# Performance work log

Hardware: AMD Instinct MI355X
Metric: run time of the kernel (lower is better)

Reference implementation:

```python
import jax, jax.numpy as jnp
import numpy as np

B, N, M = 2, 2048, 1024
C, CTX, H = 1024, 1024, 16
D = C // H
HID = int(C * 4.0)
EPS = 1e-6


def _ln(h):
    # LayerNorm32: fp32 layernorm, eps=1e-6, no affine params
    h32 = h.astype(jnp.float32)
    mu = jnp.mean(h32, axis=-1, keepdims=True)
    var = jnp.var(h32, axis=-1, keepdims=True)
    return ((h32 - mu) * jax.lax.rsqrt(var + EPS)).astype(h.dtype)


def _sdpa(q, k, v):
    # q: [B,Q,H,D], k/v: [B,K,H,D]
    scale = 1.0 / np.sqrt(D)
    s = jnp.einsum('bqhd,bkhd->bhqk', q, k) * scale
    p = jax.nn.softmax(s, axis=-1)
    return jnp.einsum('bhqk,bkhd->bqhd', p, v)


def _forward(x, context, Wqkv, bqkv, Wos, bos, Wq, bq, Wkv, bkv, Woc, boc, W1, b1, W2, b2):
    Bx, Nx, _ = x.shape
    Mx = context.shape[1]
    # --- self-attention (attn_mode='full') ---
    h = _ln(x)
    qkv = (h @ Wqkv + bqkv).reshape(Bx, Nx, 3, H, D)
    q, k, v = qkv[:, :, 0], qkv[:, :, 1], qkv[:, :, 2]
    a = _sdpa(q, k, v).reshape(Bx, Nx, C)
    x = x + (a @ Wos + bos)
    # --- cross-attention (always 'full') ---
    h = _ln(x)
    q = (h @ Wq + bq).reshape(Bx, Nx, H, D)
    kv = (context @ Wkv + bkv).reshape(Bx, Mx, 2, H, D)
    k, v = kv[:, :, 0], kv[:, :, 1]
    a = _sdpa(q, k, v).reshape(Bx, Nx, C)
    x = x + (a @ Woc + boc)
    # --- FFN with tanh-approx GELU ---
    h = _ln(x)
    x = x + (jax.nn.gelu(h @ W1 + b1, approximate=True) @ W2 + b2)
    return x


def setup_inputs() -> dict:
    key = jax.random.key(0)
    ks = jax.random.split(key, 12)
    rn = lambda k, shape: (jax.random.normal(k, shape, jnp.float32) * 0.02)
    return {
        'x': jax.random.normal(ks[0], (B, N, C), jnp.float32),
        'context': jax.random.normal(ks[1], (B, M, CTX), jnp.float32),
        'Wqkv': rn(ks[2], (C, 3 * C)), 'bqkv': jnp.zeros((3 * C,), jnp.float32),
        'Wos': rn(ks[3], (C, C)), 'bos': jnp.zeros((C,), jnp.float32),
        'Wq': rn(ks[4], (C, C)), 'bq': jnp.zeros((C,), jnp.float32),
        'Wkv': rn(ks[5], (CTX, 2 * C)), 'bkv': jnp.zeros((2 * C,), jnp.float32),
        'Woc': rn(ks[6], (C, C)), 'boc': jnp.zeros((C,), jnp.float32),
        'W1': rn(ks[7], (C, HID)), 'b1': jnp.zeros((HID,), jnp.float32),
        'W2': rn(ks[8], (HID, C)), 'b2': jnp.zeros((C,), jnp.float32),
    }


def reference(x, context, Wqkv, bqkv, Wos, bos, Wq, bq, Wkv, bkv, Woc, boc, W1, b1, W2, b2):
    return _forward(x, context, Wqkv, bqkv, Wos, bos, Wq, bq, Wkv, bkv, Woc, boc, W1, b1, W2, b2)
```

## Files before the change

kernel.cpp:

```cpp
#include <hip/hip_runtime.h>
#include <cstdint>

typedef unsigned short u16;
typedef short bf16x8 __attribute__((ext_vector_type(8)));
typedef unsigned short u16x8 __attribute__((ext_vector_type(8)));
typedef float f32x4 __attribute__((ext_vector_type(4)));

__device__ __forceinline__ u16 f2bf(float f) {
  union { float f; uint32_t u; } v; v.f = f;
  uint32_t r = (v.u + 0x7fffu + ((v.u >> 16) & 1u)) >> 16;
  return (u16)r;
}

__device__ __forceinline__ void gload_lds16(const u16* g, u16* l) {
  __builtin_amdgcn_global_load_lds(
      (const __attribute__((address_space(1))) void*)g,
      (__attribute__((address_space(3))) void*)l, 16, 0, 0);
}

__global__ __launch_bounds__(256) void ln_kernel(const float* __restrict__ x,
                                                 u16* __restrict__ h) {
  const int row = blockIdx.x;
  const int tid = threadIdx.x;
  const float4 v = *reinterpret_cast<const float4*>(x + (long)row * 1024 + tid * 4);
  float s  = v.x + v.y + v.z + v.w;
  float ss = v.x * v.x + v.y * v.y + v.z * v.z + v.w * v.w;
#pragma unroll
  for (int off = 32; off >= 1; off >>= 1) {
    s  += __shfl_xor(s, off, 64);
    ss += __shfl_xor(ss, off, 64);
  }
  __shared__ float red[8];
  const int wave = tid >> 6, lane = tid & 63;
  if (lane == 0) { red[wave] = s; red[4 + wave] = ss; }
  __syncthreads();
  s  = red[0] + red[1] + red[2] + red[3];
  ss = red[4] + red[5] + red[6] + red[7];
  const float mu   = s * (1.0f / 1024.0f);
  const float var  = ss * (1.0f / 1024.0f) - mu * mu;
  const float rstd = rsqrtf(var + 1e-6f);
  ushort4 o;
  o.x = f2bf((v.x - mu) * rstd);
  o.y = f2bf((v.y - mu) * rstd);
  o.z = f2bf((v.z - mu) * rstd);
  o.w = f2bf((v.w - mu) * rstd);
  *reinterpret_cast<ushort4*>(h + (long)row * 1024 + tid * 4) = o;
}

struct WEnt { const float* W; u16* Wt; int K, N, tEnd; };
struct WEnts { WEnt e[7]; int n; };

__global__ __launch_bounds__(256) void wconvert_all(WEnts args) {
  __shared__ u16 tile[64][72];
  int t = blockIdx.x;
  int i = 0, tStart = 0;
  while (i < args.n - 1 && t >= args.e[i].tEnd) { tStart = args.e[i].tEnd; i++; }
  const float* W = args.e[i].W;
  u16* Wt = args.e[i].Wt;
  const int K = args.e[i].K, N = args.e[i].N;
  const int rel = t - tStart;
  const int ntn = N >> 6;
  const int tn = rel % ntn, tk = rel / ntn;
  const int n0 = tn * 64, k0 = tk * 64;

  const int th = threadIdx.x;
  const int c4 = (th & 15) * 4;
  const int r  = th >> 4;
#pragma unroll
  for (int ii = 0; ii < 4; ii++) {
    const int row = ii * 16 + r;
    const float4 v = *reinterpret_cast<const float4*>(W + (long)(k0 + row) * N + n0 + c4);
    tile[c4 + 0][row] = f2bf(v.x);
    tile[c4 + 1][row] = f2bf(v.y);
    tile[c4 + 2][row] = f2bf(v.z);
    tile[c4 + 3][row] = f2bf(v.w);
  }
  __syncthreads();
  const int c8 = (th & 7) * 8;
  const int rn = th >> 3;
#pragma unroll
  for (int ii = 0; ii < 2; ii++) {
    const int row = ii * 32 + rn;
    *reinterpret_cast<u16x8*>(Wt + (long)(n0 + row) * K + k0 + c8) =
        *reinterpret_cast<const u16x8*>(&tile[row][c8]);
  }
}

__global__ __launch_bounds__(256) void f2bf_kernel(const float* __restrict__ in,
                                                   u16* __restrict__ out) {
  const long i = ((long)blockIdx.x * 256 + threadIdx.x) * 4;
  const float4 v = *reinterpret_cast<const float4*>(in + i);
  ushort4 o;
  o.x = f2bf(v.x); o.y = f2bf(v.y); o.z = f2bf(v.z); o.w = f2bf(v.w);
  *reinterpret_cast<ushort4*>(out + i) = o;
}

__global__ __launch_bounds__(256) void vtrans(const u16* __restrict__ V,
                                              u16* __restrict__ Vt,
                                              int vStride, long vBatch, int nk) {
  __shared__ u16 tile[64][72];
  const int t = threadIdx.x;
  const int b = blockIdx.z, h = blockIdx.y, n0 = blockIdx.x * 64;
  const u16* vp = V + (long)b * vBatch + h * 64;
  u16* op = Vt + (long)(b * 16 + h) * 64 * (long)nk + n0;
  const int ch = t & 7;
#pragma unroll
  for (int i = 0; i < 2; i++) {
    const int n = (t >> 3) + i * 32;
    const u16x8 v = *reinterpret_cast<const u16x8*>(vp + (long)(n0 + n) * vStride + ch * 8);
#pragma unroll
    for (int j = 0; j < 8; j++) tile[ch * 8 + j][n] = v[j];
  }
  __syncthreads();
#pragma unroll
  for (int i = 0; i < 2; i++) {
    const int d = (t >> 3) + i * 32;
    *reinterpret_cast<u16x8*>(op + (long)d * nk + ch * 8) =
        *reinterpret_cast<const u16x8*>(&tile[d][ch * 8]);
  }
}

template <int TN, int SX, bool OUT_BF16, bool GELU_ACT, bool RES, bool SPLITK = false>
__global__ __launch_bounds__(256, 2) void gemm_bt(
    const u16* __restrict__ A, const u16* __restrict__ Bt,
    const float* __restrict__ bias, const float* __restrict__ res,
    void* __restrict__ Cout, int Ndim, int Kdim, int lx, int ly) {
  constexpr int NFRAG = TN / 32;
  __shared__ u16 Al[2][128 * 32];
  __shared__ u16 Bl[2][TN * 32];
  const int j = blockIdx.x;
  const int c = j & 7, kk = j >> 3;
  const int cx = c % SX, cy = c / SX;
  const int bx = cx * lx + (kk % lx);
  const int by = cy * ly + (kk / lx);
  const int m0 = by * 128, n0 = bx * TN;

  const int tid  = threadIdx.x;
  const int lane = tid & 63, wave = tid >> 6;
  const int quad = lane >> 4, l15 = lane & 15;
  const int wr = wave >> 1, wc = wave & 1;

  f32x4 acc[4][NFRAG];
  const f32x4 vzero = {0.f, 0.f, 0.f, 0.f};
#pragma unroll
  for (int i = 0; i < 4; i++)
#pragma unroll
    for (int jj = 0; jj < NFRAG; jj++) acc[i][jj] = vzero;

  const int Keff = SPLITK ? (Kdim >> 1) : Kdim;
  const long kOff = SPLITK ? (long)blockIdx.y * Keff : 0;

  const long rowOff = (long)(lane >> 2) * Kdim + (((lane & 3) ^ ((lane >> 3) & 3)) * 8);
  const u16* gA = A  + (long)m0 * Kdim + rowOff + kOff;
  const u16* gB = Bt + (long)n0 * Kdim + rowOff + kOff;

  auto stage = [&](int k0, int p) {
    gload_lds16(gA + (long)(wave * 16) * Kdim + k0,       &Al[p][wave * 512]);
    gload_lds16(gA + (long)((wave + 4) * 16) * Kdim + k0, &Al[p][(wave + 4) * 512]);
    gload_lds16(gB + (long)(wave * 16) * Kdim + k0,       &Bl[p][wave * 512]);
    if constexpr (TN == 128)
      gload_lds16(gB + (long)((wave + 4) * 16) * Kdim + k0, &Bl[p][(wave + 4) * 512]);
  };

  const int swz = (quad ^ ((l15 >> 1) & 3)) * 8;

  stage(0, 0);
  int p = 0;
  for (int k0 = 0; k0 < Keff; k0 += 32, p ^= 1) {
    __syncthreads();
    bf16x8 af[4], bfr[NFRAG];
#pragma unroll
    for (int mt = 0; mt < 4; mt++)
      af[mt] = *reinterpret_cast<const bf16x8*>(&Al[p][(wr * 64 + mt * 16 + l15) * 32 + swz]);
#pragma unroll
    for (int nt = 0; nt < NFRAG; nt++)
      bfr[nt] = *reinterpret_cast<const bf16x8*>(&Bl[p][(wc * NFRAG * 16 + nt * 16 + l15) * 32 + swz]);
    if (k0 + 32 < Keff) stage(k0 + 32, p ^ 1);
#pragma unroll
    for (int mt = 0; mt < 4; mt++)
#pragma unroll
      for (int nt = 0; nt < NFRAG; nt++)
        acc[mt][nt] = __builtin_amdgcn_mfma_f32_16x16x32_bf16(af[mt], bfr[nt], acc[mt][nt], 0, 0, 0);
  }

#pragma unroll
  for (int nt = 0; nt < NFRAG; nt++) {
    const int col = n0 + wc * NFRAG * 16 + nt * 16 + l15;
    const float bv = bias[col];
#pragma unroll
    for (int mt = 0; mt < 4; mt++) {
#pragma unroll
      for (int r = 0; r < 4; r++) {
        const int row = m0 + wr * 64 + mt * 16 + quad * 4 + r;
        if constexpr (SPLITK) {
          float y = acc[mt][nt][r];
          if (blockIdx.y == 0) y += bv;
          unsafeAtomicAdd(&((float*)Cout)[(long)row * Ndim + col], y);
        } else {
          float y = acc[mt][nt][r] + bv;
          if (GELU_ACT) {
            const float t = 0.7978845608028654f * (y + 0.044715f * y * y * y);
            y = 0.5f * y * (1.0f + tanhf(t));
          }
          if (RES) y += res[(long)row * Ndim + col];
          if (OUT_BF16)
            ((u16*)Cout)[(long)row * Ndim + col] = f2bf(y);
          else
            ((float*)Cout)[(long)row * Ndim + col] = y;
        }
      }
    }
  }
}

__global__ __launch_bounds__(256, 2) void attn_kernel(
    const u16* __restrict__ Q, const u16* __restrict__ K, const u16* __restrict__ Vt,
    u16* __restrict__ O, int nk, int qStride, int kStride, int oStride,
    long qBatch, long kBatch, long oBatch) {
  __shared__ u16 Kt[2][64 * 64];
  __shared__ u16 Vl[2][64 * 64];
  __shared__ u16 Pl[4][32 * 64];

  const int tid = threadIdx.x;
  const int lane = tid & 63, wave = tid >> 6;
  const int quad = lane >> 4, l15 = lane & 15;
  const int b = blockIdx.z, hh = blockIdx.y, qt = blockIdx.x;

  const u16* qp = Q + (long)b * qBatch + hh * 64;
  const u16* kp = K + (long)b * kBatch + hh * 64;
  const u16* vp = Vt + (long)(b * 16 + hh) * 64 * (long)nk;

  bf16x8 qf[2][2];
  const int qrow = qt * 128 + wave * 32 + l15;
#pragma unroll
  for (int qg = 0; qg < 2; qg++) {
    qf[qg][0] = *reinterpret_cast<const bf16x8*>(qp + (long)(qrow + qg * 16) * qStride + quad * 8);
    qf[qg][1] = *reinterpret_cast<const bf16x8*>(qp + (long)(qrow + qg * 16) * qStride + 32 + quad * 8);
  }

  const int r8 = lane >> 3;
  const int gcol = ((lane & 7) ^ r8) * 8;
  const u16* kgA = kp + (long)(wave * 8 + r8) * kStride + gcol;
  const u16* kgB = kp + (long)((wave + 4) * 8 + r8) * kStride + gcol;
  const u16* vgA = vp + (long)(wave * 8 + r8) * nk + gcol;
  const u16* vgB = vp + (long)((wave + 4) * 8 + r8) * nk + gcol;

  const int cF = (quad ^ (l15 & 7)) * 8;

  const f32x4 vzero = {0.f, 0.f, 0.f, 0.f};
  f32x4 oAcc[2][4];
  float lSt[2] = {0.f, 0.f};
#pragma unroll
  for (int qg = 0; qg < 2; qg++)
#pragma unroll
    for (int i = 0; i < 4; i++) oAcc[qg][i] = vzero;

  const float SCL = 0.18033688f;
  const int nTiles = nk >> 6;
  const long kAdv = (long)64 * kStride;

  auto stage = [&](int kt, int p) {
    gload_lds16(kgA + kt * kAdv, &Kt[p][wave * 512]);
    gload_lds16(kgB + kt * kAdv, &Kt[p][(wave + 4) * 512]);
    gload_lds16(vgA + kt * 64,   &Vl[p][wave * 512]);
    gload_lds16(vgB + kt * 64,   &Vl[p][(wave + 4) * 512]);
  };

  stage(0, 0);
  int p = 0;
  for (int kt = 0; kt < nTiles; kt++, p ^= 1) {
    __syncthreads();
    if (kt + 1 < nTiles) stage(kt + 1, p ^ 1);

    f32x4 st[2][4];
#pragma unroll
    for (int mt = 0; mt < 4; mt++) {
      const bf16x8 kf0 = *reinterpret_cast<const bf16x8*>(&Kt[p][(mt * 16 + l15) * 64 + cF]);
      const bf16x8 kf1 = *reinterpret_cast<const bf16x8*>(&Kt[p][(mt * 16 + l15) * 64 + (cF ^ 32)]);
#pragma unroll
      for (int qg = 0; qg < 2; qg++) {
        f32x4 z = vzero;
        z = __builtin_amdgcn_mfma_f32_16x16x32_bf16(kf0, qf[qg][0], z, 0, 0, 0);
        z = __builtin_amdgcn_mfma_f32_16x16x32_bf16(kf1, qf[qg][1], z, 0, 0, 0);
        st[qg][mt] = z;
      }
    }

#pragma unroll
    for (int qg = 0; qg < 2; qg++) {
      float ps = 0.f;
#pragma unroll
      for (int mt = 0; mt < 4; mt++)
#pragma unroll
        for (int r = 0; r < 4; r++) {
          const float pw = __builtin_amdgcn_exp2f(st[qg][mt][r] * SCL);
          st[qg][mt][r] = pw;
          ps += pw;
        }
      lSt[qg] += ps;
      u16* plw = &Pl[wave][(qg * 16 + l15) * 64];
#pragma unroll
      for (int mt = 0; mt < 4; mt++) {
        union { float f; uint32_t u; } a0, a1, a2, a3;
        a0.f = st[qg][mt][0]; a1.f = st[qg][mt][1];
        a2.f = st[qg][mt][2]; a3.f = st[qg][mt][3];
        a0.u += 0x8000u; a1.u += 0x8000u; a2.u += 0x8000u; a3.u += 0x8000u;
        uint2 w;
        w.x = __builtin_amdgcn_perm(a1.u, a0.u, 0x07060302u);
        w.y = __builtin_amdgcn_perm(a3.u, a2.u, 0x07060302u);
        const int pcol = (((mt * 2 + (quad >> 1)) ^ (l15 & 7)) * 8) + (quad & 1) * 4;
        *reinterpret_cast<uint2*>(&plw[pcol]) = w;
      }
    }

    bf16x8 pf[2][2];
#pragma unroll
    for (int qg = 0; qg < 2; qg++) {
      const u16* plw = &Pl[wave][(qg * 16 + l15) * 64];
      pf[qg][0] = *reinterpret_cast<const bf16x8*>(&plw[cF]);
      pf[qg][1] = *reinterpret_cast<const bf16x8*>(&plw[cF ^ 32]);
    }
#pragma unroll
    for (int dt = 0; dt < 4; dt++) {
      const bf16x8 vf0 = *reinterpret_cast<const bf16x8*>(&Vl[p][(dt * 16 + l15) * 64 + cF]);
      const bf16x8 vf1 = *reinterpret_cast<const bf16x8*>(&Vl[p][(dt * 16 + l15) * 64 + (cF ^ 32)]);
#pragma unroll
      for (int qg = 0; qg < 2; qg++) {
        oAcc[qg][dt] = __builtin_amdgcn_mfma_f32_16x16x32_bf16(pf[qg][0], vf0, oAcc[qg][dt], 0, 0, 0);
        oAcc[qg][dt] = __builtin_amdgcn_mfma_f32_16x16x32_bf16(pf[qg][1], vf1, oAcc[qg][dt], 0, 0, 0);
      }
    }
  }

  u16* op = O + (long)b * oBatch + hh * 64;
#pragma unroll
  for (int qg = 0; qg < 2; qg++) {
    float l = lSt[qg];
    l += __shfl_xor(l, 16, 64);
    l += __shfl_xor(l, 32, 64);
    float lR[4];
#pragma unroll
    for (int r = 0; r < 4; r++) lR[r] = 1.0f / __shfl(l, quad * 4 + r, 64);
#pragma unroll
    for (int dt = 0; dt < 4; dt++)
#pragma unroll
      for (int r = 0; r < 4; r++) {
        const int row = qt * 128 + wave * 32 + qg * 16 + quad * 4 + r;
        op[(long)row * oStride + dt * 16 + l15] = f2bf(oAcc[qg][dt][r] * lR[r]);
      }
  }
}

extern "C" void kernel_launch(void* const* d_in, const int* in_sizes, int n_in,
                              void* d_out, int out_size, void* d_ws, size_t ws_size,
                              hipStream_t stream) {
  const float* x    = (const float*)d_in[0];
  const float* ctx  = (const float*)d_in[1];
  const float* Wqkv = (const float*)d_in[2];
  const float* bqkv = (const float*)d_in[3];
  const float* Wos  = (const float*)d_in[4];
  const float* bos  = (const float*)d_in[5];
  const float* Wq   = (const float*)d_in[6];
  const float* bq   = (const float*)d_in[7];
  const float* Wkv  = (const float*)d_in[8];
  const float* bkv  = (const float*)d_in[9];
  const float* Woc  = (const float*)d_in[10];
  const float* boc  = (const float*)d_in[11];
  const float* W1   = (const float*)d_in[12];
  const float* b1   = (const float*)d_in[13];
  const float* W2   = (const float*)d_in[14];
  const float* b2   = (const float*)d_in[15];
  float* out = (float*)d_out;
  char* ws = (char*)d_ws;
  const size_t MB = 1024 * 1024;

  if (ws_size >= 80 * MB) {
    u16* Wqkvt = (u16*)(ws + 0 * MB);
    u16* Wost  = (u16*)(ws + 6 * MB);
    u16* Wqt   = (u16*)(ws + 8 * MB);
    u16* Wkvt  = (u16*)(ws + 10 * MB);
    u16* Woct  = (u16*)(ws + 14 * MB);
    u16* W1t   = (u16*)(ws + 16 * MB);
    u16* W2t   = (u16*)(ws + 24 * MB);
    u16* h     = (u16*)(ws + 32 * MB);
    u16* abuf  = (u16*)(ws + 40 * MB);
    u16* qkv   = (u16*)(ws + 48 * MB);
    u16* q2    = (u16*)(ws + 48 * MB);
    u16* kv2   = (u16*)(ws + 56 * MB);
    u16* ctxbf = (u16*)(ws + 64 * MB);
    u16* VtCr  = (u16*)(ws + 68 * MB);
    u16* hid   = (u16*)(ws + 48 * MB);
    u16* VtSelf = h;

    WEnts we;
    we.n = 7;
    we.e[0] = {Wqkv, Wqkvt, 1024, 3072, 768};
    we.e[1] = {Wos,  Wost,  1024, 1024, 1024};
    we.e[2] = {Wq,   Wqt,   1024, 1024, 1280};
    we.e[3] = {Wkv,  Wkvt,  1024, 2048, 1792};
    we.e[4] = {Woc,  Woct,  1024, 1024, 2048};
    we.e[5] = {W1,   W1t,   1024, 4096, 3072};
    we.e[6] = {W2,   W2t,   4096, 1024, 4096};
    wconvert_all<<<dim3(4096), dim3(256), 0, stream>>>(we);
    f2bf_kernel<<<dim3(2048), dim3(256), 0, stream>>>(ctx, ctxbf);

    ln_kernel<<<dim3(4096), dim3(256), 0, stream>>>(x, h);
    gemm_bt<128, 2, true, false, false><<<dim3(768), dim3(256), 0, stream>>>(
        h, Wqkvt, bqkv, nullptr, qkv, 3072, 1024, 12, 8);
    vtrans<<<dim3(32, 16, 2), dim3(256), 0, stream>>>(
        qkv + 2048, VtSelf, 3072, (long)2048 * 3072, 2048);
    attn_kernel<<<dim3(16, 16, 2), dim3(256), 0, stream>>>(
        qkv, qkv + 1024, VtSelf, abuf, 2048, 3072, 3072, 1024,
        (long)2048 * 3072, (long)2048 * 3072, (long)2048 * 1024);
    gemm_bt<64, 1, false, false, true><<<dim3(512), dim3(256), 0, stream>>>(
        abuf, Wost, bos, x, out, 1024, 1024, 16, 4);
    ln_kernel<<<dim3(4096), dim3(256), 0, stream>>>(out, h);
    gemm_bt<64, 1, true, false, false><<<dim3(512), dim3(256), 0, stream>>>(
        h, Wqt, bq, nullptr, q2, 1024, 1024, 16, 4);
    gemm_bt<64, 2, true, false, false><<<dim3(512), dim3(256), 0, stream>>>(
        ctxbf, Wkvt, bkv, nullptr, kv2, 2048, 1024, 16, 4);
    vtrans<<<dim3(16, 16, 2), dim3(256), 0, stream>>>(
        kv2 + 1024, VtCr, 2048, (long)1024 * 2048, 1024);
    attn_kernel<<<dim3(16, 16, 2), dim3(256), 0, stream>>>(
        q2, kv2, VtCr, abuf, 1024, 1024, 2048, 1024,
        (long)2048 * 1024, (long)1024 * 2048, (long)2048 * 1024);
    gemm_bt<64, 1, false, false, true><<<dim3(512), dim3(256), 0, stream>>>(
        abuf, Woct, boc, out, out, 1024, 1024, 16, 4);
    ln_kernel<<<dim3(4096), dim3(256), 0, stream>>>(out, h);
    gemm_bt<128, 2, true, true, false><<<dim3(1024), dim3(256), 0, stream>>>(
        h, W1t, b1, nullptr, hid, 4096, 1024, 16, 8);
    gemm_bt<128, 2, false, false, false, true><<<dim3(256, 2), dim3(256), 0, stream>>>(
        hid, W2t, b2, nullptr, out, 1024, 4096, 4, 8);
  } else {
    u16* h      = (u16*)ws;
    u16* wbuf   = (u16*)(ws + 8 * MB);
    char* C0    = ws + 16 * MB;
    u16* qkv    = (u16*)C0;
    u16* Wqkvt  = (u16*)(C0 + 24 * MB);
    u16* Wost   = (u16*)C0;
    u16* q2     = (u16*)C0;
    u16* kv2    = (u16*)(C0 + 8 * MB);
    u16* Wqt    = (u16*)(C0 + 16 * MB);
    u16* Wkvt   = (u16*)(C0 + 16 * MB);
    u16* ctxbf  = (u16*)(C0 + 20 * MB);
    u16* VtCr   = (u16*)(C0 + 24 * MB);
    u16* Woct   = (u16*)(C0 + 16 * MB);
    u16* hid    = (u16*)C0;
    u16* VtSelf = h;
    u16* abuf   = wbuf;
    u16* W1t    = wbuf;
    u16* W2t    = wbuf;
    WEnts w1; w1.n = 1;

    ln_kernel<<<dim3(4096), dim3(256), 0, stream>>>(x, h);
    w1.e[0] = {Wqkv, Wqkvt, 1024, 3072, 768};
    wconvert_all<<<dim3(768), dim3(256), 0, stream>>>(w1);
    gemm_bt<128, 2, true, false, false><<<dim3(768), dim3(256), 0, stream>>>(
        h, Wqkvt, bqkv, nullptr, qkv, 3072, 1024, 12, 8);
    vtrans<<<dim3(32, 16, 2), dim3(256), 0, stream>>>(
        qkv + 2048, VtSelf, 3072, (long)2048 * 3072, 2048);
    attn_kernel<<<dim3(16, 16, 2), dim3(256), 0, stream>>>(
        qkv, qkv + 1024, VtSelf, abuf, 2048, 3072, 3072, 1024,
        (long)2048 * 3072, (long)2048 * 3072, (long)2048 * 1024);
    w1.e[0] = {Wos, Wost, 1024, 1024, 256};
    wconvert_all<<<dim3(256), dim3(256), 0, stream>>>(w1);
    gemm_bt<64, 1, false, false, true><<<dim3(512), dim3(256), 0, stream>>>(
        abuf, Wost, bos, x, out, 1024, 1024, 16, 4);
    ln_kernel<<<dim3(4096), dim3(256), 0, stream>>>(out, h);
    w1.e[0] = {Wq, Wqt, 1024, 1024, 256};
    wconvert_all<<<dim3(256), dim3(256), 0, stream>>>(w1);
    gemm_bt<64, 1, true, false, false><<<dim3(512), dim3(256), 0, stream>>>(
        h, Wqt, bq, nullptr, q2, 1024, 1024, 16, 4);
    f2bf_kernel<<<dim3(2048), dim3(256), 0, stream>>>(ctx, ctxbf);
    w1.e[0] = {Wkv, Wkvt, 1024, 2048, 512};
    wconvert_all<<<dim3(512), dim3(256), 0, stream>>>(w1);
    gemm_bt<64, 2, true, false, false><<<dim3(512), dim3(256), 0, stream>>>(
        ctxbf, Wkvt, bkv, nullptr, kv2, 2048, 1024, 16, 4);
    vtrans<<<dim3(16, 16, 2), dim3(256), 0, stream>>>(
        kv2 + 1024, VtCr, 2048, (long)1024 * 2048, 1024);
    attn_kernel<<<dim3(16, 16, 2), dim3(256), 0, stream>>>(
        q2, kv2, VtCr, abuf, 1024, 1024, 2048, 1024,
        (long)2048 * 1024, (long)1024 * 2048, (long)2048 * 1024);
    w1.e[0] = {Woc, Woct, 1024, 1024, 256};
    wconvert_all<<<dim3(256), dim3(256), 0, stream>>>(w1);
    gemm_bt<64, 1, false, false, true><<<dim3(512), dim3(256), 0, stream>>>(
        abuf, Woct, boc, out, out, 1024, 1024, 16, 4);
    ln_kernel<<<dim3(4096), dim3(256), 0, stream>>>(out, h);
    w1.e[0] = {W1, W1t, 1024, 4096, 1024};
    wconvert_all<<<dim3(1024), dim3(256), 0, stream>>>(w1);
    gemm_bt<128, 2, true, true, false><<<dim3(1024), dim3(256), 0, stream>>>(
        h, W1t, b1, nullptr, hid, 4096, 1024, 16, 8);
    w1.e[0] = {W2, W2t, 4096, 1024, 1024};
    wconvert_all<<<dim3(1024), dim3(256), 0, stream>>>(w1);
    gemm_bt<128, 2, false, false, false, true><<<dim3(256, 2), dim3(256), 0, stream>>>(
        hid, W2t, b2, nullptr, out, 1024, 4096, 4, 8);
  }
}
```

Before: 482.4 us.

## Merge Q and KV projections into one launch, batch weight converts, add split-K

Drops the large-workspace path that converted all weights once up front, and keeps a single compact path. In that path, four mid-block weight conversions are batched into one launch. The cross-attention Q projection and context KV projection now run as one dual-segment GEMM launch to fill the GPU better. The Woc output projection uses 2-way split-K with atomic accumulation into the residual, and the W2 GEMM moves from 2-way to 4-way split-K; both add parallelism but also more atomic traffic. Weight conversion now runs every call on the compact path, even when the workspace is large, which may add cost.

```diff
diff --git a/kernel.cpp b/kernel.cpp
--- a/kernel.cpp
+++ b/kernel.cpp
@@ -120,21 +120,13 @@
   }
 }
 
-template <int TN, int SX, bool OUT_BF16, bool GELU_ACT, bool RES, bool SPLITK = false>
-__global__ __launch_bounds__(256, 2) void gemm_bt(
+template <int TN, bool OUT_BF16, bool GELU_ACT, bool RES, int KSPLIT>
+__device__ __forceinline__ void gemm_core(
     const u16* __restrict__ A, const u16* __restrict__ Bt,
     const float* __restrict__ bias, const float* __restrict__ res,
-    void* __restrict__ Cout, int Ndim, int Kdim, int lx, int ly) {
+    void* __restrict__ Cout, int Ndim, int Kdim, int m0, int n0,
+    u16* Al, u16* Bl) {
   constexpr int NFRAG = TN / 32;
-  __shared__ u16 Al[2][128 * 32];
-  __shared__ u16 Bl[2][TN * 32];
-  const int j = blockIdx.x;
-  const int c = j & 7, kk = j >> 3;
-  const int cx = c % SX, cy = c / SX;
-  const int bx = cx * lx + (kk % lx);
-  const int by = cy * ly + (kk / lx);
-  const int m0 = by * 128, n0 = bx * TN;
-
   const int tid  = threadIdx.x;
   const int lane = tid & 63, wave = tid >> 6;
   const int quad = lane >> 4, l15 = lane & 15;
@@ -147,19 +139,19 @@
 #pragma unroll
     for (int jj = 0; jj < NFRAG; jj++) acc[i][jj] = vzero;
 
-  const int Keff = SPLITK ? (Kdim >> 1) : Kdim;
-  const long kOff = SPLITK ? (long)blockIdx.y * Keff : 0;
+  const int Keff = Kdim / KSPLIT;
+  const long kOff = (KSPLIT > 1) ? (long)blockIdx.y * Keff : 0;
 
   const long rowOff = (long)(lane >> 2) * Kdim + (((lane & 3) ^ ((lane >> 3) & 3)) * 8);
   const u16* gA = A  + (long)m0 * Kdim + rowOff + kOff;
   const u16* gB = Bt + (long)n0 * Kdim + rowOff + kOff;
 
   auto stage = [&](int k0, int p) {
-    gload_lds16(gA + (long)(wave * 16) * Kdim + k0,       &Al[p][wave * 512]);
-    gload_lds16(gA + (long)((wave + 4) * 16) * Kdim + k0, &Al[p][(wave + 4) * 512]);
-    gload_lds16(gB + (long)(wave * 16) * Kdim + k0,       &Bl[p][wave * 512]);
+    gload_lds16(gA + (long)(wave * 16) * Kdim + k0,       Al + p * 4096 + wave * 512);
+    gload_lds16(gA + (long)((wave + 4) * 16) * Kdim + k0, Al + p * 4096 + (wave + 4) * 512);
+    gload_lds16(gB + (long)(wave * 16) * Kdim + k0,       Bl + p * (TN * 32) + wave * 512);
     if constexpr (TN == 128)
-      gload_lds16(gB + (long)((wave + 4) * 16) * Kdim + k0, &Bl[p][(wave + 4) * 512]);
+      gload_lds16(gB + (long)((wave + 4) * 16) * Kdim + k0, Bl + p * (TN * 32) + (wave + 4) * 512);
   };
 
   const int swz = (quad ^ ((l15 >> 1) & 3)) * 8;
@@ -171,10 +163,10 @@
     bf16x8 af[4], bfr[NFRAG];
 #pragma unroll
     for (int mt = 0; mt < 4; mt++)
-      af[mt] = *reinterpret_cast<const bf16x8*>(&Al[p][(wr * 64 + mt * 16 + l15) * 32 + swz]);
+      af[mt] = *reinterpret_cast<const bf16x8*>(Al + p * 4096 + (wr * 64 + mt * 16 + l15) * 32 + swz);
 #pragma unroll
     for (int nt = 0; nt < NFRAG; nt++)
-      bfr[nt] = *reinterpret_cast<const bf16x8*>(&Bl[p][(wc * NFRAG * 16 + nt * 16 + l15) * 32 + swz]);
+      bfr[nt] = *reinterpret_cast<const bf16x8*>(Bl + p * (TN * 32) + (wc * NFRAG * 16 + nt * 16 + l15) * 32 + swz);
     if (k0 + 32 < Keff) stage(k0 + 32, p ^ 1);
 #pragma unroll
     for (int mt = 0; mt < 4; mt++)
@@ -192,7 +184,7 @@
 #pragma unroll
       for (int r = 0; r < 4; r++) {
         const int row = m0 + wr * 64 + mt * 16 + quad * 4 + r;
-        if constexpr (SPLITK) {
+        if constexpr (KSPLIT > 1) {
           float y = acc[mt][nt][r];
           if (blockIdx.y == 0) y += bv;
           unsafeAtomicAdd(&((float*)Cout)[(long)row * Ndim + col], y);
@@ -211,6 +203,43 @@
       }
     }
   }
+}
+
+template <int TN, int SX, bool OUT_BF16, bool GELU_ACT, bool RES, int KSPLIT = 1>
+__global__ __launch_bounds__(256, 2) void gemm_bt(
+    const u16* __restrict__ A, const u16* __restrict__ Bt,
+    const float* __restrict__ bias, const float* __restrict__ res,
+    void* __restrict__ Cout, int Ndim, int Kdim, int lx, int ly) {
+  __shared__ u16 Al[2 * 128 * 32];
+  __shared__ u16 Bl[2 * TN * 32];
+  const int j = blockIdx.x;
+  const int c = j & 7, kk = j >> 3;
+  const int cx = c % SX, cy = c / SX;
+  const int bx = cx * lx + (kk % lx);
+  const int by = cy * ly + (kk / lx);
+  gemm_core<TN, OUT_BF16, GELU_ACT, RES, KSPLIT>(
+      A, Bt, bias, res, Cout, Ndim, Kdim, by * 128, bx * TN, Al, Bl);
+}
+
+struct GemmSeg {
+  const u16* A; const u16* Bt; const float* bias; u16* C;
+  int Ndim, Kdim, SX, lx, ly;
+};
+struct GemmDualP { GemmSeg s0, s1; int nBlk0; };
+
+template <int TN>
+__global__ __launch_bounds__(256, 2) void gemm_dual(GemmDualP pp) {
+  __shared__ u16 Al[2 * 128 * 32];
+  __shared__ u16 Bl[2 * TN * 32];
+  int j = blockIdx.x;
+  GemmSeg s;
+  if (j < pp.nBlk0) { s = pp.s0; } else { s = pp.s1; j -= pp.nBlk0; }
+  const int c = j & 7, kk = j >> 3;
+  const int cx = c % s.SX, cy = c / s.SX;
+  const int bx = cx * s.lx + (kk % s.lx);
+  const int by = cy * s.ly + (kk / s.lx);
+  gemm_core<TN, true, false, false, 1>(
+      s.A, s.Bt, s.bias, nullptr, s.C, s.Ndim, s.Kdim, by * 128, bx * TN, Al, Bl);
 }
 
 __global__ __launch_bounds__(256, 2) void attn_kernel(
@@ -374,125 +403,69 @@
   char* ws = (char*)d_ws;
   const size_t MB = 1024 * 1024;
 
-  if (ws_size >= 80 * MB) {
-    u16* Wqkvt = (u16*)(ws + 0 * MB);
-    u16* Wost  = (u16*)(ws + 6 * MB);
-    u16* Wqt   = (u16*)(ws + 8 * MB);
-    u16* Wkvt  = (u16*)(ws + 10 * MB);
-    u16* Woct  = (u16*)(ws + 14 * MB);
-    u16* W1t   = (u16*)(ws + 16 * MB);
-    u16* W2t   = (u16*)(ws + 24 * MB);
-    u16* h     = (u16*)(ws + 32 * MB);
-    u16* abuf  = (u16*)(ws + 40 * MB);
-    u16* qkv   = (u16*)(ws + 48 * MB);
-    u16* q2    = (u16*)(ws + 48 * MB);
-    u16* kv2   = (u16*)(ws + 56 * MB);
-    u16* ctxbf = (u16*)(ws + 64 * MB);
-    u16* VtCr  = (u16*)(ws + 68 * MB);
-    u16* hid   = (u16*)(ws + 48 * MB);
-    u16* VtSelf = h;
-
-    WEnts we;
-    we.n = 7;
-    we.e[0] = {Wqkv, Wqkvt, 1024, 3072, 768};
-    we.e[1] = {Wos,  Wost,  1024, 1024, 1024};
-    we.e[2] = {Wq,   Wqt,   1024, 1024, 1280};
-    we.e[3] = {Wkv,  Wkvt,  1024, 2048, 1792};
-    we.e[4] = {Woc,  Woct,  1024, 1024, 2048};
-    we.e[5] = {W1,   W1t,   1024, 4096, 3072};
-    we.e[6] = {W2,   W2t,   4096, 1024, 4096};
-    wconvert_all<<<dim3(4096), dim3(256), 0, stream>>>(we);
-    f2bf_kernel<<<dim3(2048), dim3(256), 0, stream>>>(ctx, ctxbf);
-
-    ln_kernel<<<dim3(4096), dim3(256), 0, stream>>>(x, h);
-    gemm_bt<128, 2, true, false, false><<<dim3(768), dim3(256), 0, stream>>>(
-        h, Wqkvt, bqkv, nullptr, qkv, 3072, 1024, 12, 8);
-    vtrans<<<dim3(32, 16, 2), dim3(256), 0, stream>>>(
-        qkv + 2048, VtSelf, 3072, (long)2048 * 3072, 2048);
-    attn_kernel<<<dim3(16, 16, 2), dim3(256), 0, stream>>>(
-        qkv, qkv + 1024, VtSelf, abuf, 2048, 3072, 3072, 1024,
-        (long)2048 * 3072, (long)2048 * 3072, (long)2048 * 1024);
-    gemm_bt<64, 1, false, false, true><<<dim3(512), dim3(256), 0, stream>>>(
-        abuf, Wost, bos, x, out, 1024, 1024, 16, 4);
-    ln_kernel<<<dim3(4096), dim3(256), 0, stream>>>(out, h);
-    gemm_bt<64, 1, true, false, false><<<dim3(512), dim3(256), 0, stream>>>(
-        h, Wqt, bq, nullptr, q2, 1024, 1024, 16, 4);
-    gemm_bt<64, 2, true, false, false><<<dim3(512), dim3(256), 0, stream>>>(
-        ctxbf, Wkvt, bkv, nullptr, kv2, 2048, 1024, 16, 4);
-    vtrans<<<dim3(16, 16, 2), dim3(256), 0, stream>>>(
-        kv2 + 1024, VtCr, 2048, (long)1024 * 2048, 1024);
-    attn_kernel<<<dim3(16, 16, 2), dim3(256), 0, stream>>>(
-        q2, kv2, VtCr, abuf, 1024, 1024, 2048, 1024,
-        (long)2048 * 1024, (long)1024 * 2048, (long)2048 * 1024);
-    gemm_bt<64, 1, false, false, true><<<dim3(512), dim3(256), 0, stream>>>(
-        abuf, Woct, boc, out, out, 1024, 1024, 16, 4);
-    ln_kernel<<<dim3(4096), dim3(256), 0, stream>>>(out, h);
-    gemm_bt<128, 2, true, true, false><<<dim3(1024), dim3(256), 0, stream>>>(
-        h, W1t, b1, nullptr, hid, 4096, 1024, 16, 8);
-    gemm_bt<128, 2, false, false, false, true><<<dim3(256, 2), dim3(256), 0, stream>>>(
-        hid, W2t, b2, nullptr, out, 1024, 4096, 4, 8);
-  } else {
-    u16* h      = (u16*)ws;
-    u16* wbuf   = (u16*)(ws + 8 * MB);
-    char* C0    = ws + 16 * MB;
-    u16* qkv    = (u16*)C0;
-    u16* Wqkvt  = (u16*)(C0 + 24 * MB);
-    u16* Wost   = (u16*)C0;
-    u16* q2     = (u16*)C0;
-    u16* kv2    = (u16*)(C0 + 8 * MB);
-    u16* Wqt    = (u16*)(C0 + 16 * MB);
-    u16* Wkvt   = (u16*)(C0 + 16 * MB);
-    u16* ctxbf  = (u16*)(C0 + 20 * MB);
-    u16* VtCr   = (u16*)(C0 + 24 * MB);
-    u16* Woct   = (u16*)(C0 + 16 * MB);
-    u16* hid    = (u16*)C0;
-    u16* VtSelf = h;
-    u16* abuf   = wbuf;
-    u16* W1t    = wbuf;
-    u16* W2t    = wbuf;
-    WEnts w1; w1.n = 1;
-
-    ln_kernel<<<dim3(4096), dim3(256), 0, stream>>>(x, h);
-    w1.e[0] = {Wqkv, Wqkvt, 1024, 3072, 768};
-    wconvert_all<<<dim3(768), dim3(256), 0, stream>>>(w1);
-    gemm_bt<128, 2, true, false, false><<<dim3(768), dim3(256), 0, stream>>>(
-        h, Wqkvt, bqkv, nullptr, qkv, 3072, 1024, 12, 8);
-    vtrans<<<dim3(32, 16, 2), dim3(256), 0, stream>>>(
-        qkv + 2048, VtSelf, 3072, (long)2048 * 3072, 2048);
-    attn_kernel<<<dim3(16, 16, 2), dim3(256), 0, stream>>>(
-        qkv, qkv + 1024, VtSelf, abuf, 2048, 3072, 3072, 1024,
-        (long)2048 * 3072, (long)2048 * 3072, (long)2048 * 1024);
-    w1.e[0] = {Wos, Wost, 1024, 1024, 256};
-    wconvert_all<<<dim3(256), dim3(256), 0, stream>>>(w1);
-    gemm_bt<64, 1, false, false, true><<<dim3(512), dim3(256), 0, stream>>>(
-        abuf, Wost, bos, x, out, 1024, 1024, 16, 4);
-    ln_kernel<<<dim3(4096), dim3(256), 0, stream>>>(out, h);
-    w1.e[0] = {Wq, Wqt, 1024, 1024, 256};
-    wconvert_all<<<dim3(256), dim3(256), 0, stream>>>(w1);
-    gemm_bt<64, 1, true, false, false><<<dim3(512), dim3(256), 0, stream>>>(
-        h, Wqt, bq, nullptr, q2, 1024, 1024, 16, 4);
-    f2bf_kernel<<<dim3(2048), dim3(256), 0, stream>>>(ctx, ctxbf);
-    w1.e[0] = {Wkv, Wkvt, 1024, 2048, 512};
-    wconvert_all<<<dim3(512), dim3(256), 0, stream>>>(w1);
-    gemm_bt<64, 2, true, false, false><<<dim3(512), dim3(256), 0, stream>>>(
-        ctxbf, Wkvt, bkv, nullptr, kv2, 2048, 1024, 16, 4);
-    vtrans<<<dim3(16, 16, 2), dim3(256), 0, stream>>>(
-        kv2 + 1024, VtCr, 2048, (long)1024 * 2048, 1024);
-    attn_kernel<<<dim3(16, 16, 2), dim3(256), 0, stream>>>(
-        q2, kv2, VtCr, abuf, 1024, 1024, 2048, 1024,
-        (long)2048 * 1024, (long)1024 * 2048, (long)2048 * 1024);
-    w1.e[0] = {Woc, Woct, 1024, 1024, 256};
-    wconvert_all<<<dim3(256), dim3(256), 0, stream>>>(w1);
-    gemm_bt<64, 1, false, false, true><<<dim3(512), dim3(256), 0, stream>>>(
-        abuf, Woct, boc, out, out, 1024, 1024, 16, 4);
-    ln_kernel<<<dim3(4096), dim3(256), 0, stream>>>(out, h);
-    w1.e[0] = {W1, W1t, 1024, 4096, 1024};
-    wconvert_all<<<dim3(1024), dim3(256), 0, stream>>>(w1);
-    gemm_bt<128, 2, true, true, false><<<dim3(1024), dim3(256), 0, stream>>>(
-        h, W1t, b1, nullptr, hid, 4096, 1024, 16, 8);
-    w1.e[0] = {W2, W2t, 4096, 1024, 1024};
-    wconvert_all<<<dim3(1024), dim3(256), 0, stream>>>(w1);
-    gemm_bt<128, 2, false, false, false, true><<<dim3(256, 2), dim3(256), 0, stream>>>(
-        hid, W2t, b2, nullptr, out, 1024, 4096, 4, 8);
-  }
-}
+  u16* h      = (u16*)ws;
+  u16* abuf   = (u16*)(ws + 8 * MB);
+  u16* wbuf   = (u16*)(ws + 8 * MB);
+  u16* qkv    = (u16*)(ws + 16 * MB);
+  u16* Wqkvt  = (u16*)(ws + 40 * MB);
+  u16* Wost   = (u16*)(ws + 16 * MB);
+  u16* Wqt    = (u16*)(ws + 18 * MB);
+  u16* Wkvt   = (u16*)(ws + 20 * MB);
+  u16* Woct   = (u16*)(ws + 24 * MB);
+  u16* q2     = (u16*)(ws + 26 * MB);
+  u16* kv2    = (u16*)(ws + 34 * MB);
+  u16* ctxbf  = (u16*)(ws + 42 * MB);
+  u16* VtCr   = (u16*)(ws + 16 * MB);
+  u16* hid    = (u16*)(ws + 16 * MB);
+  u16* VtSelf = h;
+  u16* W1t    = wbuf;
+  u16* W2t    = wbuf;
+
+  WEnts w1; w1.n = 1;
+
+  ln_kernel<<<dim3(4096), dim3(256), 0, stream>>>(x, h);
+  w1.e[0] = {Wqkv, Wqkvt, 1024, 3072, 768};
+  wconvert_all<<<dim3(768), dim3(256), 0, stream>>>(w1);
+  gemm_bt<128, 2, true, false, false><<<dim3(768), dim3(256), 0, stream>>>(
+      h, Wqkvt, bqkv, nullptr, qkv, 3072, 1024, 12, 8);
+  vtrans<<<dim3(32, 16, 2), dim3(256), 0, stream>>>(
+      qkv + 2048, VtSelf, 3072, (long)2048 * 3072, 2048);
+  attn_kernel<<<dim3(16, 16, 2), dim3(256), 0, stream>>>(
+      qkv, qkv + 1024, VtSelf, abuf, 2048, 3072, 3072, 1024,
+      (long)2048 * 3072, (long)2048 * 3072, (long)2048 * 1024);
+
+  WEnts w4; w4.n = 4;
+  w4.e[0] = {Wos, Wost, 1024, 1024, 256};
+  w4.e[1] = {Wq,  Wqt,  1024, 1024, 512};
+  w4.e[2] = {Wkv, Wkvt, 1024, 2048, 1024};
+  w4.e[3] = {Woc, Woct, 1024, 1024, 1280};
+  wconvert_all<<<dim3(1280), dim3(256), 0, stream>>>(w4);
+  f2bf_kernel<<<dim3(2048), dim3(256), 0, stream>>>(ctx, ctxbf);
+
+  gemm_bt<64, 1, false, false, true><<<dim3(512), dim3(256), 0, stream>>>(
+      abuf, Wost, bos, x, out, 1024, 1024, 16, 4);
+  ln_kernel<<<dim3(4096), dim3(256), 0, stream>>>(out, h);
+
+  GemmDualP dp;
+  dp.s0 = {h,     Wqt,  bq,  q2,  1024, 1024, 1, 16, 4};
+  dp.s1 = {ctxbf, Wkvt, bkv, kv2, 2048, 1024, 2, 16, 4};
+  dp.nBlk0 = 512;
+  gemm_dual<64><<<dim3(1024), dim3(256), 0, stream>>>(dp);
+  vtrans<<<dim3(16, 16, 2), dim3(256), 0, stream>>>(
+      kv2 + 1024, VtCr, 2048, (long)1024 * 2048, 1024);
+  attn_kernel<<<dim3(16, 16, 2), dim3(256), 0, stream>>>(
+      q2, kv2, VtCr, abuf, 1024, 1024, 2048, 1024,
+      (long)2048 * 1024, (long)1024 * 2048, (long)2048 * 1024);
+  gemm_bt<64, 1, false, false, false, 2><<<dim3(512, 2), dim3(256), 0, stream>>>(
+      abuf, Woct, boc, nullptr, out, 1024, 1024, 16, 4);
+
+  ln_kernel<<<dim3(4096), dim3(256), 0, stream>>>(out, h);
+  w1.e[0] = {W1, W1t, 1024, 4096, 1024};
+  wconvert_all<<<dim3(1024), dim3(256), 0, stream>>>(w1);
+  gemm_bt<128, 2, true, true, false><<<dim3(1024), dim3(256), 0, stream>>>(
+      h, W1t, b1, nullptr, hid, 4096, 1024, 16, 8);
+  w1.e[0] = {W2, W2t, 4096, 1024, 1024};
+  wconvert_all<<<dim3(1024), dim3(256), 0, stream>>>(w1);
+  gemm_bt<128, 2, false, false, false, 4><<<dim3(256, 4), dim3(256), 0, stream>>>(
+      hid, W2t, b2, nullptr, out, 1024, 4096, 4, 8);
+}
```

Measured after the change: 520.9 us. 1.08x slower.
